# Kernel optimization log

Hardware: AMD Instinct MI355X
Metric: run time of the kernel (lower is better)

The kernel has to match this reference:

```python
import jax, jax.numpy as jnp
import numpy as np

C_M, C_Z, C_H = 256, 128, 32
S, N = 128, 384
EPS = 1e-5


def setup_inputs() -> dict:
    key = jax.random.key(0)
    ks = jax.random.split(key, 8)
    sc = 1.0 / np.sqrt(C_M)
    return {
        "msa": jax.random.normal(ks[0], (S, N, C_M), dtype=jnp.float32),
        "ln_g": jnp.ones((C_M,), dtype=jnp.float32),
        "ln_b": jnp.zeros((C_M,), dtype=jnp.float32),
        "Wl": jax.random.uniform(ks[1], (C_M, C_H), jnp.float32, -sc, sc),
        "bl": jax.random.uniform(ks[2], (C_H,), jnp.float32, -sc, sc),
        "Wr": jax.random.uniform(ks[3], (C_M, C_H), jnp.float32, -sc, sc),
        "br": jax.random.uniform(ks[4], (C_H,), jnp.float32, -sc, sc),
        "Wo": jax.random.uniform(ks[5], (C_H * C_H, C_Z), jnp.float32, -1.0 / C_H, 1.0 / C_H),
        "bo": jax.random.uniform(ks[6], (C_Z,), jnp.float32, -1.0 / C_H, 1.0 / C_H),
    }


def _layernorm(x, g, b):
    mu = jnp.mean(x, axis=-1, keepdims=True)
    var = jnp.mean(jnp.square(x - mu), axis=-1, keepdims=True)
    return (x - mu) * jax.lax.rsqrt(var + EPS) * g + b


def reference(msa, ln_g, ln_b, Wl, bl, Wr, br, Wo, bo):
    s = msa.shape[0]
    m = _layernorm(msa, ln_g, ln_b)          # [s, n, c_m]
    left = m @ Wl + bl                        # [s, n, c_h]
    right = m @ Wr + br                       # [s, n, c_h]
    outer = jnp.einsum('sic,sjd->ijcd', left, right) / s  # [n, n, c_h, c_h]
    outer = outer.reshape(outer.shape[0], outer.shape[1], -1)
    return outer @ Wo + bo                    # [n, n, c_z]
```

## Files before the change

### kernel.cpp

```cpp
#include <hip/hip_runtime.h>
#include <hip/hip_bf16.h>

#define CM 256
#define CZ 128
#define CH 32
#define SS 128
#define NN 384

typedef short bf16x8 __attribute__((ext_vector_type(8)));
typedef float f32x4 __attribute__((ext_vector_type(4)));
typedef unsigned short us4 __attribute__((ext_vector_type(4)));
typedef unsigned short us8 __attribute__((ext_vector_type(8)));

__device__ __forceinline__ unsigned short f2bf(float f) {
    __hip_bfloat16 h = __float2bfloat16(f);
    return __builtin_bit_cast(unsigned short, h);
}

__global__ __launch_bounds__(256) void k0_transpose(
    const float* __restrict__ Wo, const float* __restrict__ Wl, const float* __restrict__ Wr,
    unsigned short* __restrict__ WoF, unsigned short* __restrict__ WT) {
    int n = blockIdx.x;
    int base = n * 1024;
#pragma unroll
    for (int u = 0; u < 4; u++) {
        int w   = base + u * 256 + threadIdx.x;
        int e   = w & 7;
        int l   = (w >> 3) & 63;
        int zb  = (w >> 9) & 7;
        int cch = w >> 12;
        WoF[w] = f2bf(Wo[(size_t)(cch * 32 + (l >> 4) * 8 + e) * CZ + zb * 16 + (l & 15)]);
    }
    int k = threadIdx.x;
    if (n < 32) {
        WT[n * CM + k] = f2bf(Wl[(size_t)k * CH + n]);
    } else if (n < 64) {
        WT[32 * CM + (n - 32) * CM + k] = f2bf(Wr[(size_t)k * CH + (n - 32)]);
    }
}

__global__ __launch_bounds__(256, 2) void k1_ln_proj(
    const float* __restrict__ msa, const float* __restrict__ g, const float* __restrict__ bta,
    const unsigned short* __restrict__ WT, const float* __restrict__ bl, const float* __restrict__ br,
    unsigned short* __restrict__ Lt, unsigned short* __restrict__ Rt)
{
    __shared__ unsigned short A_lds[64 * 264];
    __shared__ unsigned short B_lds[64 * 264];

    const int i    = blockIdx.x;
    const int sh   = blockIdx.y;
    const int t    = threadIdx.x;
    const int wv   = t >> 6;
    const int lane = t & 63;
    const int lr   = lane & 15, lg = lane >> 4;

    const float4 gv = ((const float4*)g)[lane];
    const float4 bv = ((const float4*)bta)[lane];
#pragma unroll 8
    for (int r = 0; r < 16; r++) {
        int sl = wv * 16 + r;
        int s  = sh * 64 + sl;
        float4 v = ((const float4*)(msa + ((size_t)s * NN + i) * CM))[lane];
        float sum = v.x + v.y + v.z + v.w;
        float sq  = v.x * v.x + v.y * v.y + v.z * v.z + v.w * v.w;
#pragma unroll
        for (int off = 32; off >= 1; off >>= 1) {
            sum += __shfl_xor(sum, off, 64);
            sq  += __shfl_xor(sq, off, 64);
        }
        float mu = sum * (1.f / CM);
        float rs = rsqrtf(sq * (1.f / CM) - mu * mu + 1e-5f);
        us4 pk;
        pk[0] = f2bf((v.x - mu) * rs * gv.x + bv.x);
        pk[1] = f2bf((v.y - mu) * rs * gv.y + bv.y);
        pk[2] = f2bf((v.z - mu) * rs * gv.z + bv.z);
        pk[3] = f2bf((v.w - mu) * rs * gv.w + bv.w);
        *(us4*)&A_lds[sl * 264 + lane * 4] = pk;
    }
#pragma unroll
    for (int u = 0; u < 8; u++) {
        int id = u * 256 + t;
        *(us8*)&B_lds[(id >> 5) * 264 + (id & 31) * 8] = *(const us8*)&WT[id * 8];
    }
    __syncthreads();

    const int m0 = (wv >> 1) * 32;
    const int n0 = (wv & 1) * 32;
    f32x4 acc[2][2];
#pragma unroll
    for (int a = 0; a < 2; a++)
#pragma unroll
        for (int b = 0; b < 2; b++) acc[a][b] = (f32x4){0.f, 0.f, 0.f, 0.f};

#pragma unroll
    for (int ks = 0; ks < 8; ks++) {
        int ko = ks * 32 + lg * 8;
        bf16x8 a0 = *(const bf16x8*)&A_lds[(m0 + lr) * 264 + ko];
        bf16x8 a1 = *(const bf16x8*)&A_lds[(m0 + 16 + lr) * 264 + ko];
        bf16x8 b0 = *(const bf16x8*)&B_lds[(n0 + lr) * 264 + ko];
        bf16x8 b1 = *(const bf16x8*)&B_lds[(n0 + 16 + lr) * 264 + ko];
        acc[0][0] = __builtin_amdgcn_mfma_f32_16x16x32_bf16(a0, b0, acc[0][0], 0, 0, 0);
        acc[0][1] = __builtin_amdgcn_mfma_f32_16x16x32_bf16(a0, b1, acc[0][1], 0, 0, 0);
        acc[1][0] = __builtin_amdgcn_mfma_f32_16x16x32_bf16(a1, b0, acc[1][0], 0, 0, 0);
        acc[1][1] = __builtin_amdgcn_mfma_f32_16x16x32_bf16(a1, b1, acc[1][1], 0, 0, 0);
    }

    const bool isL = (n0 == 0);
    const float scale = isL ? 0.0078125f : 1.f;
#pragma unroll
    for (int mt = 0; mt < 2; mt++)
#pragma unroll
        for (int nt = 0; nt < 2; nt++) {
            int ch = (n0 + nt * 16 + lr) & 31;
            float bias = isL ? bl[ch] : br[ch];
            us4 pk;
#pragma unroll
            for (int rg = 0; rg < 4; rg++)
                pk[rg] = f2bf((acc[mt][nt][rg] + bias) * scale);
            unsigned short* dst = (isL ? Lt : Rt) + (size_t)(i * CH + ch) * SS
                                  + sh * 64 + m0 + mt * 16 + lg * 4;
            *(us4*)dst = pk;
        }
}

#define TI 8
#define TJ 8
#define OH1_OFF  65536
#define K2_LDS   139264

__global__ __launch_bounds__(512, 2) void k2_fused(
    const unsigned short* __restrict__ Lt, const unsigned short* __restrict__ Rt,
    const unsigned short* __restrict__ WoF, const float* __restrict__ bo,
    float* __restrict__ out)
{
    extern __shared__ char smem[];
    unsigned short* A = (unsigned short*)(smem);

    const int i0 = blockIdx.x * TI;
    const int j0 = blockIdx.y * TJ;
    const int t  = threadIdx.x;
    const int wv = t >> 6, lane = t & 63;
    const int lr = lane & 15, lg = lane >> 4;

    const int m0  = (wv >> 2) * 128;
    const int n0w = (wv & 3) * 64;

    const unsigned short* gA = Lt + (size_t)i0 * CH * SS;
    const unsigned short* gB = Rt + (size_t)j0 * CH * SS;

    us8 rA[8];
#pragma unroll
    for (int u = 0; u < 8; u++) {
        int c = u * 512 + t;
        rA[u] = *(const us8*)(gA + (c >> 4) * 128 + (c & 15) * 8);
    }
    bf16x8 breg[16];
#pragma unroll
    for (int nt = 0; nt < 4; nt++)
#pragma unroll
        for (int ks = 0; ks < 4; ks++)
            breg[nt * 4 + ks] = *(const bf16x8*)(gB + (n0w + nt * 16 + lr) * 128 + (ks * 4 + lg) * 8);
#pragma unroll
    for (int u = 0; u < 8; u++) {
        int c = u * 512 + t;
        *(us8*)(A + (c >> 4) * 136 + (c & 15) * 8) = rA[u];
    }
    __syncthreads();

    f32x4 accE[4][4], accO[4][4];
#pragma unroll
    for (int a = 0; a < 4; a++)
#pragma unroll
        for (int b = 0; b < 4; b++) {
            accE[a][b] = (f32x4){0.f, 0.f, 0.f, 0.f};
            accO[a][b] = (f32x4){0.f, 0.f, 0.f, 0.f};
        }

#pragma unroll
    for (int ks = 0; ks < 4; ks++) {
        int ko = ks * 32 + lg * 8;
#pragma unroll
        for (int mt = 0; mt < 8; mt++) {
            bf16x8 af = *(const bf16x8*)&A[(m0 + mt * 16 + lr) * 136 + ko];
#pragma unroll
            for (int nt = 0; nt < 4; nt++) {
                if (mt & 1)
                    accO[mt >> 1][nt] = __builtin_amdgcn_mfma_f32_16x16x32_bf16(breg[nt * 4 + ks], af, accO[mt >> 1][nt], 0, 0, 0);
                else
                    accE[mt >> 1][nt] = __builtin_amdgcn_mfma_f32_16x16x32_bf16(breg[nt * 4 + ks], af, accE[mt >> 1][nt], 0, 0, 0);
            }
        }
    }

    const int zsl = wv & 1, ksl = wv >> 1;

    bf16x8 wbuf[4][4];
#pragma unroll
    for (int pc = 0; pc < 4; pc++)
#pragma unroll
        for (int bi = 0; bi < 4; bi++)
            wbuf[pc][bi] = *(const bf16x8*)&WoF[(((size_t)(pc * 4 + ksl) * 8 + zsl * 4 + bi) * 64 + lane) * 8];

    __syncthreads();

    {
        unsigned short* Oh0 = (unsigned short*)smem;
        unsigned short* Oh1 = (unsigned short*)(smem + OH1_OFF);
#pragma unroll
        for (int mh = 0; mh < 4; mh++) {
            int iiw  = (wv >> 2) * 4 + mh;
            int rowH = iiw * 16 + lr;
            int okey = (rowH ^ (rowH >> 4)) & 7;
#pragma unroll
            for (int nt = 0; nt < 4; nt++) {
                int colBase = n0w + nt * 16 + lg * 4;
                int chk = (colBase >> 3) ^ okey;
                int off = rowH * 256 + chk * 8 + (lg & 1) * 4;
                us4 pkE, pkO;
#pragma unroll
                for (int rg = 0; rg < 4; rg++) {
                    pkE[rg] = f2bf(accE[mh][nt][rg]);
                    pkO[rg] = f2bf(accO[mh][nt][rg]);
                }
                *(us4*)&Oh0[off] = pkE;
                *(us4*)&Oh1[off] = pkO;
            }
        }
    }
    __syncthreads();

    f32x4 acc2[4][4];
#pragma unroll
    for (int a = 0; a < 4; a++)
#pragma unroll
        for (int b = 0; b < 4; b++) acc2[a][b] = (f32x4){0.f, 0.f, 0.f, 0.f};

#pragma unroll
    for (int c = 0; c < 8; c++) {
        const int cch = c * 4 + ksl;
        const int hh  = cch >> 4;
        const int cH  = cch & 15;
        const unsigned short* OhX = (const unsigned short*)(smem + (hh ? OH1_OFF : 0));

        bf16x8 af2[4];
#pragma unroll
        for (int ai = 0; ai < 4; ai++) {
            int rowH = (ai * 2 + ((lane >> 3) & 1)) * 16 + cH;
            int okey = (rowH ^ (rowH >> 4)) & 7;
            int chk  = (((lane & 7) * 4 + lg) ^ okey);
            af2[ai] = *(const bf16x8*)&OhX[rowH * 256 + chk * 8];
        }
#pragma unroll
        for (int ai = 0; ai < 4; ai++)
#pragma unroll
            for (int bi = 0; bi < 4; bi++)
                acc2[ai][bi] = __builtin_amdgcn_mfma_f32_16x16x32_bf16(af2[ai], wbuf[c & 3][bi], acc2[ai][bi], 0, 0, 0);

        if (c < 4) {
            int cchn = (c + 4) * 4 + ksl;
#pragma unroll
            for (int bi = 0; bi < 4; bi++)
                wbuf[c & 3][bi] = *(const bf16x8*)&WoF[(((size_t)cchn * 8 + zsl * 4 + bi) * 64 + lane) * 8];
        }
    }
    __syncthreads();

    float* RB = (float*)smem;
#pragma unroll
    for (int ai = 0; ai < 4; ai++)
#pragma unroll
        for (int bi = 0; bi < 4; bi++) {
            int z  = zsl * 64 + bi * 16 + lr;
            int pr = ai * 16 + lg * 4;
            *(f32x4*)&RB[ksl * 8704 + z * 68 + pr] = acc2[ai][bi];
        }
    __syncthreads();

    {
        int z = t >> 2, pq = t & 3;
        float bz = bo[z];
#pragma unroll
        for (int u = 0; u < 4; u++) {
            int p0r = pq * 16 + u * 4;
            f32x4 s = (f32x4){0.f, 0.f, 0.f, 0.f};
#pragma unroll
            for (int ks2 = 0; ks2 < 4; ks2++)
                s += *(const f32x4*)&RB[ks2 * 8704 + z * 68 + p0r];
#pragma unroll
            for (int e = 0; e < 4; e++) {
                int p = p0r + e;
                out[((size_t)(i0 + (p >> 3)) * NN + (j0 + (p & 7))) * CZ + z] = s[e] + bz;
            }
        }
    }
}

extern "C" void kernel_launch(void* const* d_in, const int* in_sizes, int n_in,
                              void* d_out, int out_size, void* d_ws, size_t ws_size,
                              hipStream_t stream) {
    const float* msa  = (const float*)d_in[0];
    const float* ln_g = (const float*)d_in[1];
    const float* ln_b = (const float*)d_in[2];
    const float* Wl   = (const float*)d_in[3];
    const float* bl   = (const float*)d_in[4];
    const float* Wr   = (const float*)d_in[5];
    const float* br   = (const float*)d_in[6];
    const float* Wo   = (const float*)d_in[7];
    const float* bo   = (const float*)d_in[8];
    float* out = (float*)d_out;

    unsigned short* Lt  = (unsigned short*)d_ws;
    unsigned short* Rt  = Lt + (size_t)NN * CH * SS;
    unsigned short* WoF = Rt + (size_t)NN * CH * SS;
    unsigned short* WT  = WoF + (size_t)CZ * CH * CH;

    hipFuncSetAttribute((const void*)k2_fused,
                        hipFuncAttributeMaxDynamicSharedMemorySize, K2_LDS);

    k0_transpose<<<dim3(CZ), dim3(256), 0, stream>>>(Wo, Wl, Wr, WoF, WT);
    k1_ln_proj<<<dim3(NN, 2), dim3(256), 0, stream>>>(msa, ln_g, ln_b, WT, bl, br, Lt, Rt);
    k2_fused<<<dim3(NN / TI, NN / TJ), dim3(512), K2_LDS, stream>>>(Lt, Rt, WoF, bo, out);
}
```

Baseline: 229.9 us.

## Store L/R in MFMA-fragment tiled layout and load A via direct global-to-LDS

Changes the intermediate Lt/Rt layout written by the projection kernel into 16-row x 8-element fragment tiles that match the MFMA operand layout. The fused outer-product kernel then copies the A tile straight from global memory into LDS with global_load_lds, skipping the register staging and the padded LDS write. B fragments and A fragment reads become contiguous 16-byte accesses, and A fragments for a k-step are batched before the MFMAs. The cost is an unpadded LDS layout whose bank-conflict behaviour now depends on the fragment tiling, plus an explicit vmcnt wait.

```diff
diff --git a/kernel.cpp b/kernel.cpp
--- a/kernel.cpp
+++ b/kernel.cpp
@@ -15,6 +15,13 @@
 __device__ __forceinline__ unsigned short f2bf(float f) {
     __hip_bfloat16 h = __float2bfloat16(f);
     return __builtin_bit_cast(unsigned short, h);
+}
+
+__device__ __forceinline__ void gl_lds16(const unsigned short* g, unsigned short* l) {
+    __builtin_amdgcn_global_load_lds(
+        (const __attribute__((address_space(1))) unsigned int*)g,
+        (__attribute__((address_space(3))) unsigned int*)l,
+        16, 0, 0);
 }
 
 __global__ __launch_bounds__(256) void k0_transpose(
@@ -117,8 +124,10 @@
 #pragma unroll
             for (int rg = 0; rg < 4; rg++)
                 pk[rg] = f2bf((acc[mt][nt][rg] + bias) * scale);
-            unsigned short* dst = (isL ? Lt : Rt) + (size_t)(i * CH + ch) * SS
-                                  + sh * 64 + m0 + mt * 16 + lg * 4;
+            int s0 = sh * 64 + m0 + mt * 16 + lg * 4;
+            int rt = i * 2 + (ch >> 4);
+            unsigned short* dst = (isL ? Lt : Rt)
+                + (size_t)rt * 2048 + (s0 >> 3) * 128 + (ch & 15) * 8 + (s0 & 7);
             *(us4*)dst = pk;
         }
 }
@@ -145,26 +154,21 @@
     const int m0  = (wv >> 2) * 128;
     const int n0w = (wv & 3) * 64;
 
-    const unsigned short* gA = Lt + (size_t)i0 * CH * SS;
-    const unsigned short* gB = Rt + (size_t)j0 * CH * SS;
-
-    us8 rA[8];
-#pragma unroll
-    for (int u = 0; u < 8; u++) {
-        int c = u * 512 + t;
-        rA[u] = *(const us8*)(gA + (c >> 4) * 128 + (c & 15) * 8);
+    const unsigned short* gA = Lt + (size_t)i0 * 4096;
+    const unsigned short* gB = Rt + (size_t)j0 * 4096;
+
+#pragma unroll
+    for (int p = 0; p < 8; p++) {
+        int q = wv * 8 + p;
+        gl_lds16(gA + q * 512 + lane * 8, A + q * 512);
     }
     bf16x8 breg[16];
 #pragma unroll
     for (int nt = 0; nt < 4; nt++)
 #pragma unroll
         for (int ks = 0; ks < 4; ks++)
-            breg[nt * 4 + ks] = *(const bf16x8*)(gB + (n0w + nt * 16 + lr) * 128 + (ks * 4 + lg) * 8);
-#pragma unroll
-    for (int u = 0; u < 8; u++) {
-        int c = u * 512 + t;
-        *(us8*)(A + (c >> 4) * 136 + (c & 15) * 8) = rA[u];
-    }
+            breg[nt * 4 + ks] = *(const bf16x8*)&gB[((n0w >> 4) + nt) * 2048 + ks * 512 + lg * 128 + lr * 8];
+    asm volatile("s_waitcnt vmcnt(0)" ::: "memory");
     __syncthreads();
 
     f32x4 accE[4][4], accO[4][4];
@@ -178,18 +182,19 @@
 
 #pragma unroll
     for (int ks = 0; ks < 4; ks++) {
-        int ko = ks * 32 + lg * 8;
-#pragma unroll
-        for (int mt = 0; mt < 8; mt++) {
-            bf16x8 af = *(const bf16x8*)&A[(m0 + mt * 16 + lr) * 136 + ko];
+        bf16x8 af[8];
+#pragma unroll
+        for (int mt = 0; mt < 8; mt++)
+            af[mt] = *(const bf16x8*)&A[((m0 >> 4) + mt) * 2048 + ks * 512 + lg * 128 + lr * 8];
+#pragma unroll
+        for (int mt = 0; mt < 8; mt++)
 #pragma unroll
             for (int nt = 0; nt < 4; nt++) {
                 if (mt & 1)
-                    accO[mt >> 1][nt] = __builtin_amdgcn_mfma_f32_16x16x32_bf16(breg[nt * 4 + ks], af, accO[mt >> 1][nt], 0, 0, 0);
+                    accO[mt >> 1][nt] = __builtin_amdgcn_mfma_f32_16x16x32_bf16(breg[nt * 4 + ks], af[mt], accO[mt >> 1][nt], 0, 0, 0);
                 else
-                    accE[mt >> 1][nt] = __builtin_amdgcn_mfma_f32_16x16x32_bf16(breg[nt * 4 + ks], af, accE[mt >> 1][nt], 0, 0, 0);
+                    accE[mt >> 1][nt] = __builtin_amdgcn_mfma_f32_16x16x32_bf16(breg[nt * 4 + ks], af[mt], accE[mt >> 1][nt], 0, 0, 0);
             }
-        }
     }
 
     const int zsl = wv & 1, ksl = wv >> 1;
```

New measurement: 214.9 us. 1.07x faster.
